# Optimization experiments

Hardware: AMD Instinct MI355X
Metric: run time of the kernel (lower is better)

Reference implementation:

```python
import jax, jax.numpy as jnp
import numpy as np

EPS = 1e-5

def _layer_norm(x, gamma, beta):
    # LayerNorm over the last two dims [C, 128], matching nn.LayerNorm([C, 128])
    mean = jnp.mean(x, axis=(-2, -1), keepdims=True)
    var = jnp.var(x, axis=(-2, -1), keepdims=True)
    return (x - mean) * jax.lax.rsqrt(var + EPS) * gamma + beta


def setup_inputs() -> dict:
    key = jax.random.key(0)
    ks = jax.random.split(key, 7)
    B, C, N, L = 64, 1024, 128, 512
    W_SCALE = 0.02  # keep pre-softmax logits / activations in a sane range
    return {
        "X_in": jax.random.normal(ks[0], (B, C, N), jnp.float32),
        "T": jax.random.normal(ks[1], (B, C, L), jnp.float32),
        "Wq": jax.random.normal(ks[2], (C, C), jnp.float32) * W_SCALE,
        "Wk": jax.random.normal(ks[3], (C, C), jnp.float32) * W_SCALE,
        "Wv": jax.random.normal(ks[4], (C, C), jnp.float32) * W_SCALE,
        "Wf1": jax.random.normal(ks[5], (C, C), jnp.float32) * W_SCALE,
        "Wf2": jax.random.normal(ks[6], (C, C), jnp.float32) * W_SCALE,
        "gamma": jnp.ones((C, N), jnp.float32),
        "beta": jnp.zeros((C, N), jnp.float32),
    }


def reference(X_in, T, Wq, Wk, Wv, Wf1, Wf2, gamma, beta):
    C = Wq.shape[1]  # feature_map_cs (intended value of the buggy X_in.weight.shape[1])
    # 1x1 Conv1d == per-position channel matmul: weight [out, in]
    q = jnp.einsum('oc,bcn->bon', Wq, X_in)      # [B, C, N]
    k = jnp.einsum('oc,bcl->bol', Wk, T)         # [B, C, L]
    sim = jnp.einsum('bcn,bcl->bnl', q, k) / jnp.sqrt(jnp.float32(C))  # [B, N, L]
    attn = jax.nn.softmax(sim, axis=2)           # softmax over tokens L
    v = jnp.einsum('oc,bcl->bol', Wv, T)         # [B, C, L]
    ctx = jnp.einsum('bcl,bnl->bcn', v, attn)    # [B, C, N] == bmm(values, attn^T)
    X_out = _layer_norm(X_in + ctx, gamma, beta)
    h = jax.nn.relu(jnp.einsum('oc,bcn->bon', Wf1, X_out))
    ffn = jnp.einsum('oc,bcn->bon', Wf2, h)
    return _layer_norm(X_out + ffn, gamma, beta)
```

## Files before the change

### kernel.cpp

```cpp
#include <hip/hip_runtime.h>


using bf16   = __bf16;
using bf16x4 = __attribute__((ext_vector_type(4))) __bf16;
using bf16x8 = __attribute__((ext_vector_type(8))) __bf16;
using f32x4  = __attribute__((ext_vector_type(4))) float;

static constexpr int  Bb = 64;
static constexpr int  Cc = 1024;
static constexpr int  Nn = 128;
static constexpr int  Ll = 512;
static constexpr long long PLANE = (long long)Cc * Nn;
static constexpr float INV_PLANE = 1.0f / 131072.0f;

__device__ __forceinline__ void gload_lds16(const void* g, void* l) {
    __builtin_amdgcn_global_load_lds(
        (__attribute__((address_space(1))) void*)g,
        (__attribute__((address_space(3))) void*)l,
        16, 0, 0);
}

__global__ void __launch_bounds__(256)
prep_all(const float* __restrict__ Wv, const float* __restrict__ Wf1,
         const float* __restrict__ Wf2, const float* __restrict__ Wq,
         const float* __restrict__ Wk, const float* __restrict__ X,
         const float* __restrict__ T,
         bf16* __restrict__ WvB, bf16* __restrict__ Wf1B, bf16* __restrict__ Wf2B,
         bf16* __restrict__ WqT, bf16* __restrict__ WkT,
         bf16* __restrict__ Xt, bf16* __restrict__ Tt, bf16* __restrict__ Tb) {
    __shared__ float tile[64][65];
    const int bx = blockIdx.x;
    const int t  = threadIdx.x;
    if (bx < 3072) {
        const float* in = bx < 1024 ? Wv : (bx < 2048 ? Wf1 : Wf2);
        bf16* out       = bx < 1024 ? WvB : (bx < 2048 ? Wf1B : Wf2B);
        int i = (bx & 1023) * 256 + t;
        float4 v = reinterpret_cast<const float4*>(in)[i];
        bf16x4 o = { (bf16)v.x, (bf16)v.y, (bf16)v.z, (bf16)v.w };
        reinterpret_cast<bf16x4*>(out)[i] = o;
        return;
    }
    const float* in; bf16* outT; bf16* outS = nullptr;
    int R, S, bxx, byy, bz = 0;
    if (bx < 3584) {
        int j = bx - 3072;
        in = (j >= 256) ? Wk : Wq; outT = (j >= 256) ? WkT : WqT;
        R = Cc; S = Cc; j &= 255; bxx = j & 15; byy = j >> 4;
    } else if (bx < 5632) {
        int j = bx - 3584; bz = j >> 5; j &= 31;
        bxx = j & 1; byy = j >> 1; in = X; outT = Xt; R = Cc; S = Nn;
    } else {
        int j = bx - 5632; bz = j >> 7; j &= 127;
        bxx = j & 7; byy = j >> 3; in = T; outT = Tt; outS = Tb; R = Cc; S = Ll;
    }
    long long plane = (long long)R * S;
    in   += (long long)bz * plane;
    outT += (long long)bz * plane;
    if (outS) outS += (long long)bz * plane;
    int s0 = bxx * 64, r0 = byy * 64;
    int rl = t >> 4;
    int sc = (t & 15) * 4;
    #pragma unroll
    for (int p = 0; p < 4; ++p) {
        int r = p * 16 + rl;
        float4 v = *(const float4*)(in + (long long)(r0 + r) * S + s0 + sc);
        *(float4*)&tile[r][sc] = v;
        if (outS) {
            bf16x4 o = { (bf16)v.x, (bf16)v.y, (bf16)v.z, (bf16)v.w };
            *(bf16x4*)(outS + (long long)(r0 + r) * S + s0 + sc) = o;
        }
    }
    __syncthreads();
    int sb = t >> 3;
    int rg = (t & 7) * 8;
    #pragma unroll
    for (int p = 0; p < 2; ++p) {
        int s = sb + p * 32;
        bf16x8 o;
        #pragma unroll
        for (int j = 0; j < 8; ++j) o[j] = (bf16)tile[rg + j][s];
        *(bf16x8*)(outT + (long long)(s0 + s) * R + r0 + rg) = o;
    }
}

#define GEMM_PROLOGUE_AND_LOOP(A_, Bt_, K_)                                        \
    __shared__ bf16 As[2][128 * 64];                                               \
    __shared__ bf16 Bs[2][128 * 64];                                               \
    const int n0   = blockIdx.x * 128;                                             \
    const int m0   = blockIdx.y * 128;                                             \
    const int t    = threadIdx.x;                                                  \
    const int lane = t & 63;                                                       \
    const int w    = t >> 6;                                                       \
    const int wr   = (w >> 1) * 64;                                                \
    const int wc   = (w & 1) * 64;                                                 \
    const int lr   = lane & 15;                                                    \
    const int hi4  = (lane >> 4) * 16;                                             \
    const int sw   = (lr & 7) << 4;                                                \
    const bf16* gA[4]; const bf16* gB[4]; int lo[4];                               \
    _Pragma("unroll")                                                              \
    for (int p = 0; p < 4; ++p) {                                                  \
        int o = w * 1024 + lane * 16 + p * 4096;                                   \
        int row = o >> 7;                                                          \
        int scol = ((o & 127) ^ ((row & 7) << 4)) >> 1;                            \
        lo[p] = o;                                                                 \
        gA[p] = A_  + (long long)(m0 + row) * K_ + scol;                           \
        gB[p] = Bt_ + (long long)(n0 + row) * K_ + scol;                           \
    }                                                                              \
    f32x4 acc[4][4] = {};                                                          \
    const int NT_ = K_ / 64;                                                       \
    _Pragma("unroll")                                                              \
    for (int p = 0; p < 4; ++p) gload_lds16(gA[p], (char*)As[0] + lo[p]);          \
    _Pragma("unroll")                                                              \
    for (int p = 0; p < 4; ++p) gload_lds16(gB[p], (char*)Bs[0] + lo[p]);          \
    __syncthreads();                                                               \
    int cur_ = 0;                                                                  \
    for (int kt = 0; kt < NT_; ++kt) {                                             \
        if (kt + 1 < NT_) {                                                        \
            _Pragma("unroll")                                                      \
            for (int p = 0; p < 4; ++p)                                            \
                gload_lds16(gA[p] + (kt + 1) * 64, (char*)As[cur_ ^ 1] + lo[p]);   \
            _Pragma("unroll")                                                      \
            for (int p = 0; p < 4; ++p)                                            \
                gload_lds16(gB[p] + (kt + 1) * 64, (char*)Bs[cur_ ^ 1] + lo[p]);   \
        }                                                                          \
        const bf16* As_ = As[cur_]; const bf16* Bs_ = Bs[cur_];                    \
        _Pragma("unroll")                                                          \
        for (int kk = 0; kk < 2; ++kk) {                                           \
            bf16x8 af[4], bfr[4];                                                  \
            _Pragma("unroll")                                                      \
            for (int i = 0; i < 4; ++i) {                                          \
                int ra = wr + i * 16 + lr;                                         \
                int rb = wc + i * 16 + lr;                                         \
                af[i]  = *(const bf16x8*)((const char*)As_ +                       \
                          ((((ra << 7) + (kk << 6) + hi4)) ^ sw));                 \
                bfr[i] = *(const bf16x8*)((const char*)Bs_ +                       \
                          ((((rb << 7) + (kk << 6) + hi4)) ^ sw));                 \
            }                                                                      \
            _Pragma("unroll")                                                      \
            for (int mi = 0; mi < 4; ++mi)                                         \
                _Pragma("unroll")                                                  \
                for (int ni = 0; ni < 4; ++ni)                                     \
                    acc[mi][ni] = __builtin_amdgcn_mfma_f32_16x16x32_bf16(         \
                        af[mi], bfr[ni], acc[mi][ni], 0, 0, 0);                    \
        }                                                                          \
        __syncthreads();                                                           \
        cur_ ^= 1;                                                                 \
    }

template <typename OutT, bool RELU>
__global__ void __launch_bounds__(256, 2)
gemm_tn(const bf16* __restrict__ A, const bf16* __restrict__ Bt, OutT* __restrict__ C,
        int M, int N, int K, long long sA, long long sBt, long long sC, float scale) {
    A  += (long long)blockIdx.z * sA;
    Bt += (long long)blockIdx.z * sBt;
    C  += (long long)blockIdx.z * sC;
    GEMM_PROLOGUE_AND_LOOP(A, Bt, K)
    const int rbase = m0 + wr + (lane >> 4) * 4;
    const int cbase = n0 + wc + lr;
    #pragma unroll
    for (int mi = 0; mi < 4; ++mi)
        #pragma unroll
        for (int ni = 0; ni < 4; ++ni)
            #pragma unroll
            for (int r = 0; r < 4; ++r) {
                float v = acc[mi][ni][r] * scale;
                if (RELU) v = fmaxf(v, 0.0f);
                C[(long long)(rbase + mi * 16 + r) * N + (cbase + ni * 16)] = (OutT)v;
            }
}

__global__ void __launch_bounds__(256, 2)
gemm_sim_exp(const bf16* __restrict__ A , const bf16* __restrict__ Bt ,
             bf16* __restrict__ E, float* __restrict__ rspart, int K,
             long long sA, long long sBt) {
    A  += (long long)blockIdx.z * sA;
    Bt += (long long)blockIdx.z * sBt;
    E  += (long long)blockIdx.z * ((long long)Nn * Ll);
    GEMM_PROLOGUE_AND_LOOP(A, Bt, K)
    const int rbase = m0 + wr + (lane >> 4) * 4;
    const int cbase = n0 + wc + lr;
    __shared__ float rs[2][128];
    float psum[4][4];
    #pragma unroll
    for (int mi = 0; mi < 4; ++mi)
        #pragma unroll
        for (int r = 0; r < 4; ++r) psum[mi][r] = 0.f;
    #pragma unroll
    for (int mi = 0; mi < 4; ++mi)
        #pragma unroll
        for (int ni = 0; ni < 4; ++ni)
            #pragma unroll
            for (int r = 0; r < 4; ++r) {
                float ev = __expf(acc[mi][ni][r] * 0.03125f);
                E[(long long)(rbase + mi * 16 + r) * Ll + (cbase + ni * 16)] = (bf16)ev;
                psum[mi][r] += ev;
            }
    #pragma unroll
    for (int mi = 0; mi < 4; ++mi)
        #pragma unroll
        for (int r = 0; r < 4; ++r) {
            float v = psum[mi][r];
            v += __shfl_xor(v, 1); v += __shfl_xor(v, 2);
            v += __shfl_xor(v, 4); v += __shfl_xor(v, 8);
            psum[mi][r] = v;
        }
    if (lr == 0) {
        #pragma unroll
        for (int mi = 0; mi < 4; ++mi)
            #pragma unroll
            for (int r = 0; r < 4; ++r)
                rs[wc ? 1 : 0][wr + (lane >> 4) * 4 + mi * 16 + r] = psum[mi][r];
    }
    __syncthreads();
    if (t < 128)
        rspart[((long long)blockIdx.z * 4 + blockIdx.x) * 128 + t] = rs[0][t] + rs[1][t];
}

__global__ void __launch_bounds__(256, 2)
gemm_u_scaled(const bf16* __restrict__ A , const bf16* __restrict__ Bt ,
              bf16* __restrict__ C, const float* __restrict__ rspart, int K,
              long long sA, long long sBt, long long sC) {
    A  += (long long)blockIdx.z * sA;
    Bt += (long long)blockIdx.z * sBt;
    C  += (long long)blockIdx.z * sC;
    const float* rp = rspart + (long long)blockIdx.z * 512;
    GEMM_PROLOGUE_AND_LOOP(A, Bt, K)
    const int rbase = m0 + wr + (lane >> 4) * 4;
    const int cbase = n0 + wc + lr;
    #pragma unroll
    for (int mi = 0; mi < 4; ++mi)
        #pragma unroll
        for (int r = 0; r < 4; ++r) {
            int row = rbase + mi * 16 + r;
            float inv = 1.f / (rp[row] + rp[128 + row] + rp[256 + row] + rp[384 + row]);
            #pragma unroll
            for (int ni = 0; ni < 4; ++ni)
                C[(long long)row * Cc + (cbase + ni * 16)] = (bf16)(acc[mi][ni][r] * inv);
        }
}

__global__ void __launch_bounds__(256, 2)
gemm_ctx_ln1(const bf16* __restrict__ A , const bf16* __restrict__ Bt ,
             const float* __restrict__ X, bf16* __restrict__ Z1, float* __restrict__ partials,
             int K, long long sBt) {
    const int N = Nn;
    Bt += (long long)blockIdx.z * sBt;
    X  += (long long)blockIdx.z * PLANE;
    Z1 += (long long)blockIdx.z * PLANE;
    GEMM_PROLOGUE_AND_LOOP(A, Bt, K)
    const int rbase = m0 + wr + (lane >> 4) * 4;
    const int cbase = n0 + wc + lr;
    float s = 0.f, ss = 0.f;
    #pragma unroll
    for (int mi = 0; mi < 4; ++mi)
        #pragma unroll
        for (int ni = 0; ni < 4; ++ni)
            #pragma unroll
            for (int r = 0; r < 4; ++r) {
                long long idx = (long long)(rbase + mi * 16 + r) * N + (cbase + ni * 16);
                float zv = acc[mi][ni][r] + X[idx];
                Z1[idx] = (bf16)zv;
                s += zv; ss += zv * zv;
            }
    #pragma unroll
    for (int off = 32; off; off >>= 1) { s += __shfl_xor(s, off); ss += __shfl_xor(ss, off); }
    __shared__ float red[8];
    if (lane == 0) { red[w] = s; red[4 + w] = ss; }
    __syncthreads();
    if (t == 0) {
        float S = red[0] + red[1] + red[2] + red[3];
        float SS = red[4] + red[5] + red[6] + red[7];
        float* p = partials + ((long long)blockIdx.z * 8 + blockIdx.y) * 2;
        p[0] = S; p[1] = SS;
    }
}

__global__ void __launch_bounds__(256, 2)
gemm_ffn_ln2(const bf16* __restrict__ A , const bf16* __restrict__ Bt ,
             const bf16* __restrict__ Z1, const float* __restrict__ pp1,
             const float* __restrict__ gamma, const float* __restrict__ beta,
             bf16* __restrict__ Z2, float* __restrict__ partials,
             int K, long long sA) {
    A  += (long long)blockIdx.z * sA;
    Z1 += (long long)blockIdx.z * PLANE;
    Z2 += (long long)blockIdx.z * PLANE;
    float S1 = 0.f, SS1 = 0.f;
    #pragma unroll
    for (int j = 0; j < 8; ++j) {
        S1  += pp1[((long long)blockIdx.z * 8 + j) * 2];
        SS1 += pp1[((long long)blockIdx.z * 8 + j) * 2 + 1];
    }
    const float mean1 = S1 * INV_PLANE;
    const float rstd1 = rsqrtf(SS1 * INV_PLANE - mean1 * mean1 + 1e-5f);
    GEMM_PROLOGUE_AND_LOOP(A, Bt, K)
    const int rbase = m0 + wr + (lane >> 4) * 4;
    const int cbase = n0 + wc + lr;
    float s = 0.f, ss = 0.f;
    #pragma unroll
    for (int mi = 0; mi < 4; ++mi)
        #pragma unroll
        for (int ni = 0; ni < 4; ++ni) {
            long long a = (long long)(cbase + ni * 16) * Nn + rbase + mi * 16;
            bf16x4 z1v = *(const bf16x4*)(Z1 + a);
            float4 g  = *(const float4*)(gamma + a);
            float4 be = *(const float4*)(beta + a);
            float x0 = ((float)z1v[0] - mean1) * rstd1 * g.x + be.x;
            float x1 = ((float)z1v[1] - mean1) * rstd1 * g.y + be.y;
            float x2 = ((float)z1v[2] - mean1) * rstd1 * g.z + be.z;
            float x3 = ((float)z1v[3] - mean1) * rstd1 * g.w + be.w;
            float z0 = acc[mi][ni][0] + x0, z1 = acc[mi][ni][1] + x1;
            float z2 = acc[mi][ni][2] + x2, z3 = acc[mi][ni][3] + x3;
            bf16x4 zo = { (bf16)z0, (bf16)z1, (bf16)z2, (bf16)z3 };
            *(bf16x4*)(Z2 + a) = zo;
            s  += z0 + z1 + z2 + z3;
            ss += z0 * z0 + z1 * z1 + z2 * z2 + z3 * z3;
        }
    #pragma unroll
    for (int off = 32; off; off >>= 1) { s += __shfl_xor(s, off); ss += __shfl_xor(ss, off); }
    __shared__ float red[8];
    if (lane == 0) { red[w] = s; red[4 + w] = ss; }
    __syncthreads();
    if (t == 0) {
        float S = red[0] + red[1] + red[2] + red[3];
        float SS = red[4] + red[5] + red[6] + red[7];
        float* p = partials + ((long long)blockIdx.z * 8 + blockIdx.x) * 2;
        p[0] = S; p[1] = SS;
    }
}

__global__ void ln1_norm_transpose(const bf16* __restrict__ Z1, const float* __restrict__ partials,
                                   const float* __restrict__ gamma, const float* __restrict__ beta,
                                   bf16* __restrict__ XoutT) {
    int b = blockIdx.z;
    float S = 0.f, SS = 0.f;
    #pragma unroll
    for (int j = 0; j < 8; ++j) {
        S  += partials[((long long)b * 8 + j) * 2];
        SS += partials[((long long)b * 8 + j) * 2 + 1];
    }
    float mean = S * INV_PLANE;
    float var  = SS * INV_PLANE - mean * mean;
    float rstd = rsqrtf(var + 1e-5f);
    __shared__ float tile[64][65];
    long long base = (long long)b * PLANE;
    int n0 = blockIdx.x * 64, c0 = blockIdx.y * 64;
    int t = threadIdx.x;
    int rl = t >> 4;
    int sc = (t & 15) * 4;
    #pragma unroll
    for (int p = 0; p < 4; ++p) {
        int r = p * 16 + rl;
        long long idx = (long long)(c0 + r) * Nn + n0 + sc;
        bf16x4 z  = *(const bf16x4*)(Z1 + base + idx);
        float4 g  = *(const float4*)(gamma + idx);
        float4 be = *(const float4*)(beta + idx);
        float4 o = {((float)z[0] - mean) * rstd * g.x + be.x,
                    ((float)z[1] - mean) * rstd * g.y + be.y,
                    ((float)z[2] - mean) * rstd * g.z + be.z,
                    ((float)z[3] - mean) * rstd * g.w + be.w};
        *(float4*)&tile[r][sc] = o;
    }
    __syncthreads();
    int sb = t >> 3;
    int rg = (t & 7) * 8;
    #pragma unroll
    for (int p = 0; p < 2; ++p) {
        int n = sb + p * 32;
        bf16x8 o;
        #pragma unroll
        for (int j = 0; j < 8; ++j) o[j] = (bf16)tile[rg + j][n];
        *(bf16x8*)(XoutT + base + (long long)(n0 + n) * Cc + c0 + rg) = o;
    }
}

__global__ void ln2_final(const bf16* __restrict__ Z2, const float* __restrict__ partials,
                          const float* __restrict__ gamma, const float* __restrict__ beta,
                          float* __restrict__ out) {
    int b = blockIdx.y;
    float S = 0.f, SS = 0.f;
    #pragma unroll
    for (int j = 0; j < 8; ++j) {
        S  += partials[((long long)b * 8 + j) * 2];
        SS += partials[((long long)b * 8 + j) * 2 + 1];
    }
    float mean = S * INV_PLANE;
    float var  = SS * INV_PLANE - mean * mean;
    float rstd = rsqrtf(var + 1e-5f);
    long long base = (long long)b * PLANE;
    int i = (blockIdx.x * 256 + threadIdx.x) * 8;
    bf16x8 z = *(const bf16x8*)(Z2 + base + i);
    #pragma unroll
    for (int h = 0; h < 2; ++h) {
        float4 g  = *(const float4*)(gamma + i + h * 4);
        float4 be = *(const float4*)(beta + i + h * 4);
        float4 o = {((float)z[h * 4 + 0] - mean) * rstd * g.x + be.x,
                    ((float)z[h * 4 + 1] - mean) * rstd * g.y + be.y,
                    ((float)z[h * 4 + 2] - mean) * rstd * g.z + be.z,
                    ((float)z[h * 4 + 3] - mean) * rstd * g.w + be.w};
        *(float4*)(out + base + i + h * 4) = o;
    }
}

extern "C" void kernel_launch(void* const* d_in, const int* in_sizes, int n_in,
                              void* d_out, int out_size, void* d_ws, size_t ws_size,
                              hipStream_t stream) {
    const float* X   = (const float*)d_in[0];
    const float* T   = (const float*)d_in[1];
    const float* Wq  = (const float*)d_in[2];
    const float* Wk  = (const float*)d_in[3];
    const float* Wv  = (const float*)d_in[4];
    const float* Wf1 = (const float*)d_in[5];
    const float* Wf2 = (const float*)d_in[6];
    const float* gamma = (const float*)d_in[7];
    const float* beta  = (const float*)d_in[8];
    float* out = (float*)d_out;
    char* ws = (char*)d_ws;
    const size_t MB = 1ull << 20;

    bf16* WvB  = (bf16*)(ws + 0 * MB);
    bf16* Wf1B = (bf16*)(ws + 2 * MB);
    bf16* Wf2B = (bf16*)(ws + 4 * MB);
    bf16* WqT  = (bf16*)(ws + 6 * MB);
    bf16* WkT  = (bf16*)(ws + 8 * MB);
    bf16* G2   = (bf16*)(ws + 10 * MB);
    bf16* Xt   = (bf16*)(ws + 12 * MB);
    bf16* Tt   = (bf16*)(ws + 28 * MB);
    bf16* Z1   = (bf16*)(ws + 28 * MB);
    bf16* Tb   = (bf16*)(ws + 92 * MB);
    bf16* XoutT= (bf16*)(ws + 92 * MB);
    bf16* hT   = (bf16*)(ws + 108 * MB);
    bf16* e    = (bf16*)(ws + 156 * MB);
    bf16* Z2   = (bf16*)(ws + 156 * MB);
    bf16* E    = (bf16*)(ws + 188 * MB);
    bf16* u    = (bf16*)(ws + 196 * MB);
    float* pp1 = (float*)(ws + 212 * MB);
    float* pp2 = (float*)(ws + 212 * MB + 65536);
    float* rsp = (float*)(ws + 213 * MB);

    dim3 blk256(256);

    prep_all<<<dim3(13824), blk256, 0, stream>>>(
        Wv, Wf1, Wf2, Wq, Wk, X, T, WvB, Wf1B, Wf2B, WqT, WkT, Xt, Tt, Tb);

    gemm_tn<bf16, false><<<dim3(8, 8, 1), blk256, 0, stream>>>(
        WkT, WqT, G2, Cc, Cc, Cc, 0, 0, 0, 1.f);
    gemm_tn<bf16, false><<<dim3(8, 1, Bb), blk256, 0, stream>>>(
        Xt, G2, e, Nn, Cc, Cc, (long long)Nn * Cc, 0, (long long)Nn * Cc, 1.f);
    gemm_sim_exp<<<dim3(4, 1, Bb), blk256, 0, stream>>>(
        e, Tt, E, rsp, Cc, (long long)Nn * Cc, (long long)Ll * Cc);
    gemm_u_scaled<<<dim3(8, 1, Bb), blk256, 0, stream>>>(
        E, Tb, u, rsp, Ll, (long long)Nn * Ll, (long long)Cc * Ll, (long long)Nn * Cc);
    gemm_ctx_ln1<<<dim3(1, 8, Bb), blk256, 0, stream>>>(
        WvB, u, X, Z1, pp1, Cc, (long long)Nn * Cc);
    ln1_norm_transpose<<<dim3(Nn / 64, Cc / 64, Bb), blk256, 0, stream>>>(
        Z1, pp1, gamma, beta, XoutT);
    gemm_tn<bf16, true><<<dim3(8, 1, Bb), blk256, 0, stream>>>(
        XoutT, Wf1B, hT, Nn, Cc, Cc, (long long)Nn * Cc, 0, (long long)Nn * Cc, 1.f);
    gemm_ffn_ln2<<<dim3(8, 1, Bb), blk256, 0, stream>>>(
        hT, Wf2B, Z1, pp1, gamma, beta, Z2, pp2, Cc, (long long)Nn * Cc);
    ln2_final<<<dim3(64, Bb), blk256, 0, stream>>>(Z2, pp2, gamma, beta, out);
}
```

Before: 291.8 us.

## Store transposed bf16 operands in 64x64 tiled blocks for contiguous GEMM tile loads

The transpose kernels now write their bf16 outputs as contiguous 64x64 blocks (4096 elements) instead of row-major, and the GEMM prologue gains template flags so tiled operands are addressed by block with a 4096-element K step. Each 64-wide K slice of a 64-row group then comes from one contiguous 8 KB region, which should improve DRAM/TLB locality for the global-to-LDS loads. The change adds producer/consumer coupling. Any consumer of these buffers that still assumes row-major layout would read wrong data.

```diff
diff --git a/kernel.cpp b/kernel.cpp
--- a/kernel.cpp
+++ b/kernel.cpp
@@ -71,6 +71,7 @@
         }
     }
     __syncthreads();
+    long long tb = ((long long)(s0 >> 6) * (R >> 6) + (r0 >> 6)) * 4096;
     int sb = t >> 3;
     int rg = (t & 7) * 8;
     #pragma unroll
@@ -79,11 +80,11 @@
         bf16x8 o;
         #pragma unroll
         for (int j = 0; j < 8; ++j) o[j] = (bf16)tile[rg + j][s];
-        *(bf16x8*)(outT + (long long)(s0 + s) * R + r0 + rg) = o;
-    }
-}
-
-#define GEMM_PROLOGUE_AND_LOOP(A_, Bt_, K_)                                        \
+        *(bf16x8*)(outT + tb + s * 64 + rg) = o;
+    }
+}
+
+#define GEMM_PROLOGUE_AND_LOOP(A_, Bt_, K_, TA_, TB_)                              \
     __shared__ bf16 As[2][128 * 64];                                               \
     __shared__ bf16 Bs[2][128 * 64];                                               \
     const int n0   = blockIdx.x * 128;                                             \
@@ -96,6 +97,8 @@
     const int lr   = lane & 15;                                                    \
     const int hi4  = (lane >> 4) * 16;                                             \
     const int sw   = (lr & 7) << 4;                                                \
+    const int stepA_ = (TA_) ? 4096 : 64;                                          \
+    const int stepB_ = (TB_) ? 4096 : 64;                                          \
     const bf16* gA[4]; const bf16* gB[4]; int lo[4];                               \
     _Pragma("unroll")                                                              \
     for (int p = 0; p < 4; ++p) {                                                  \
@@ -103,8 +106,13 @@
         int row = o >> 7;                                                          \
         int scol = ((o & 127) ^ ((row & 7) << 4)) >> 1;                            \
         lo[p] = o;                                                                 \
-        gA[p] = A_  + (long long)(m0 + row) * K_ + scol;                           \
-        gB[p] = Bt_ + (long long)(n0 + row) * K_ + scol;                           \
+        int ra = m0 + row, rb = n0 + row;                                          \
+        gA[p] = (TA_) ? A_ + ((long long)(ra >> 6) * (K_ >> 6)) * 4096             \
+                           + (ra & 63) * 64 + scol                                 \
+                      : A_ + (long long)ra * K_ + scol;                            \
+        gB[p] = (TB_) ? Bt_ + ((long long)(rb >> 6) * (K_ >> 6)) * 4096            \
+                            + (rb & 63) * 64 + scol                                \
+                      : Bt_ + (long long)rb * K_ + scol;                           \
     }                                                                              \
     f32x4 acc[4][4] = {};                                                          \
     const int NT_ = K_ / 64;                                                       \
@@ -118,10 +126,12 @@
         if (kt + 1 < NT_) {                                                        \
             _Pragma("unroll")                                                      \
             for (int p = 0; p < 4; ++p)                                            \
-                gload_lds16(gA[p] + (kt + 1) * 64, (char*)As[cur_ ^ 1] + lo[p]);   \
+                gload_lds16(gA[p] + (long long)(kt + 1) * stepA_,                  \
+                            (char*)As[cur_ ^ 1] + lo[p]);                          \
             _Pragma("unroll")                                                      \
             for (int p = 0; p < 4; ++p)                                            \
-                gload_lds16(gB[p] + (kt + 1) * 64, (char*)Bs[cur_ ^ 1] + lo[p]);   \
+                gload_lds16(gB[p] + (long long)(kt + 1) * stepB_,                  \
+                            (char*)Bs[cur_ ^ 1] + lo[p]);                          \
         }                                                                          \
         const bf16* As_ = As[cur_]; const bf16* Bs_ = Bs[cur_];                    \
         _Pragma("unroll")                                                          \
@@ -147,14 +157,14 @@
         cur_ ^= 1;                                                                 \
     }
 
-template <typename OutT, bool RELU>
+template <typename OutT, bool RELU, int TA, int TB>
 __global__ void __launch_bounds__(256, 2)
 gemm_tn(const bf16* __restrict__ A, const bf16* __restrict__ Bt, OutT* __restrict__ C,
         int M, int N, int K, long long sA, long long sBt, long long sC, float scale) {
     A  += (long long)blockIdx.z * sA;
     Bt += (long long)blockIdx.z * sBt;
     C  += (long long)blockIdx.z * sC;
-    GEMM_PROLOGUE_AND_LOOP(A, Bt, K)
+    GEMM_PROLOGUE_AND_LOOP(A, Bt, K, TA, TB)
     const int rbase = m0 + wr + (lane >> 4) * 4;
     const int cbase = n0 + wc + lr;
     #pragma unroll
@@ -176,7 +186,7 @@
     A  += (long long)blockIdx.z * sA;
     Bt += (long long)blockIdx.z * sBt;
     E  += (long long)blockIdx.z * ((long long)Nn * Ll);
-    GEMM_PROLOGUE_AND_LOOP(A, Bt, K)
+    GEMM_PROLOGUE_AND_LOOP(A, Bt, K, 0, 1)
     const int rbase = m0 + wr + (lane >> 4) * 4;
     const int cbase = n0 + wc + lr;
     __shared__ float rs[2][128];
@@ -224,7 +234,7 @@
     Bt += (long long)blockIdx.z * sBt;
     C  += (long long)blockIdx.z * sC;
     const float* rp = rspart + (long long)blockIdx.z * 512;
-    GEMM_PROLOGUE_AND_LOOP(A, Bt, K)
+    GEMM_PROLOGUE_AND_LOOP(A, Bt, K, 0, 0)
     const int rbase = m0 + wr + (lane >> 4) * 4;
     const int cbase = n0 + wc + lr;
     #pragma unroll
@@ -247,7 +257,7 @@
     Bt += (long long)blockIdx.z * sBt;
     X  += (long long)blockIdx.z * PLANE;
     Z1 += (long long)blockIdx.z * PLANE;
-    GEMM_PROLOGUE_AND_LOOP(A, Bt, K)
+    GEMM_PROLOGUE_AND_LOOP(A, Bt, K, 0, 0)
     const int rbase = m0 + wr + (lane >> 4) * 4;
     const int cbase = n0 + wc + lr;
     float s = 0.f, ss = 0.f;
@@ -292,7 +302,7 @@
     }
     const float mean1 = S1 * INV_PLANE;
     const float rstd1 = rsqrtf(SS1 * INV_PLANE - mean1 * mean1 + 1e-5f);
-    GEMM_PROLOGUE_AND_LOOP(A, Bt, K)
+    GEMM_PROLOGUE_AND_LOOP(A, Bt, K, 0, 0)
     const int rbase = m0 + wr + (lane >> 4) * 4;
     const int cbase = n0 + wc + lr;
     float s = 0.f, ss = 0.f;
@@ -361,6 +371,7 @@
         *(float4*)&tile[r][sc] = o;
     }
     __syncthreads();
+    long long tb = ((long long)(n0 >> 6) * (Cc >> 6) + (c0 >> 6)) * 4096;
     int sb = t >> 3;
     int rg = (t & 7) * 8;
     #pragma unroll
@@ -369,7 +380,7 @@
         bf16x8 o;
         #pragma unroll
         for (int j = 0; j < 8; ++j) o[j] = (bf16)tile[rg + j][n];
-        *(bf16x8*)(XoutT + base + (long long)(n0 + n) * Cc + c0 + rg) = o;
+        *(bf16x8*)(XoutT + base + tb + n * 64 + rg) = o;
     }
 }
 
@@ -442,9 +453,9 @@
     prep_all<<<dim3(13824), blk256, 0, stream>>>(
         Wv, Wf1, Wf2, Wq, Wk, X, T, WvB, Wf1B, Wf2B, WqT, WkT, Xt, Tt, Tb);
 
-    gemm_tn<bf16, false><<<dim3(8, 8, 1), blk256, 0, stream>>>(
+    gemm_tn<bf16, false, 1, 1><<<dim3(8, 8, 1), blk256, 0, stream>>>(
         WkT, WqT, G2, Cc, Cc, Cc, 0, 0, 0, 1.f);
-    gemm_tn<bf16, false><<<dim3(8, 1, Bb), blk256, 0, stream>>>(
+    gemm_tn<bf16, false, 1, 0><<<dim3(8, 1, Bb), blk256, 0, stream>>>(
         Xt, G2, e, Nn, Cc, Cc, (long long)Nn * Cc, 0, (long long)Nn * Cc, 1.f);
     gemm_sim_exp<<<dim3(4, 1, Bb), blk256, 0, stream>>>(
         e, Tt, E, rsp, Cc, (long long)Nn * Cc, (long long)Ll * Cc);
@@ -454,7 +465,7 @@
         WvB, u, X, Z1, pp1, Cc, (long long)Nn * Cc);
     ln1_norm_transpose<<<dim3(Nn / 64, Cc / 64, Bb), blk256, 0, stream>>>(
         Z1, pp1, gamma, beta, XoutT);
-    gemm_tn<bf16, true><<<dim3(8, 1, Bb), blk256, 0, stream>>>(
+    gemm_tn<bf16, true, 1, 0><<<dim3(8, 1, Bb), blk256, 0, stream>>>(
         XoutT, Wf1B, hT, Nn, Cc, Cc, (long long)Nn * Cc, 0, (long long)Nn * Cc, 1.f);
     gemm_ffn_ln2<<<dim3(8, 1, Bb), blk256, 0, stream>>>(
         hT, Wf2B, Z1, pp1, gamma, beta, Z2, pp2, Cc, (long long)Nn * Cc);
```

After: 293.3 us. No clear change (+0.5%).
